# Kernel tuning notes

Measured on AMD Instinct MI355X. Metric: run time of the kernel, lower is better.

## Reference

```python
import jax, jax.numpy as jnp
import numpy as np
from jax import lax

B, W, RSS, NLED, LED_F, HID = 8192, 512, 12, 16, 8, 64


def setup_inputs() -> dict:
    key = jax.random.key(0)
    ks = jax.random.split(key, 20)
    s = 0.05
    return {
        "rss_chunk": jax.random.normal(ks[0], (B, W, RSS), jnp.float32),
        "anchor_pos": jax.random.normal(ks[1], (B, 3), jnp.float32),
        "led_feats": jax.random.normal(ks[2], (NLED, LED_F), jnp.float32),
        "led_positions": jax.random.normal(ks[3], (NLED, 3), jnp.float32),
        "freq_mask": jax.random.randint(ks[4], (RSS, NLED), 0, 2, jnp.int32),
        # temporal_conv params (torch Conv1d weight layout [out, in, k])
        "conv1_w": jax.random.normal(ks[5], (32, RSS, 3), jnp.float32) * s,
        "conv1_b": jax.random.normal(ks[6], (32,), jnp.float32) * s,
        "conv2_w": jax.random.normal(ks[7], (64, 32, 3), jnp.float32) * s,
        "conv2_b": jax.random.normal(ks[8], (64,), jnp.float32) * s,
        # projections (torch Linear weight layout [out, in])
        "q_w": jax.random.normal(ks[9], (64, W + 3), jnp.float32) * s,
        "q_b": jax.random.normal(ks[10], (64,), jnp.float32) * s,
        "k_w": jax.random.normal(ks[11], (64, LED_F + 3), jnp.float32) * s,
        "k_b": jax.random.normal(ks[12], (64,), jnp.float32) * s,
        "red_w": jax.random.normal(ks[13], (64, RSS * LED_F), jnp.float32) * s,
        "red_b": jax.random.normal(ks[14], (64,), jnp.float32) * s,
        "fus_w": jax.random.normal(ks[15], (HID, 64 + 64), jnp.float32) * s,
        "fus_b": jax.random.normal(ks[16], (HID,), jnp.float32) * s,
    }


def _conv1d(x, w, b, stride):
    # x: [B, C_in, L], w: [C_out, C_in, k], padding 1
    y = lax.conv_general_dilated(x, w, (stride,), [(1, 1)],
                                 dimension_numbers=("NCH", "OIH", "NCH"))
    return y + b[None, :, None]


def reference(rss_chunk, anchor_pos, led_feats, led_positions, freq_mask,
              conv1_w, conv1_b, conv2_w, conv2_b,
              q_w, q_b, k_w, k_b, red_w, red_b, fus_w, fus_b):
    Bc = rss_chunk.shape[0]
    x = jnp.swapaxes(rss_chunk, 1, 2)                       # [B, 12, W]

    # temporal conv branch -> [B, 64]
    h = jax.nn.relu(_conv1d(x, conv1_w, conv1_b, 1))        # [B, 32, W]
    h = jax.nn.relu(_conv1d(h, conv2_w, conv2_b, 2))        # [B, 64, W//2]
    t_feat = h.mean(axis=-1)                                # AdaptiveAvgPool1d(1)

    # queries: [B, 12, W+3] -> [B, 12, 64]
    pos_rep = jnp.broadcast_to(anchor_pos[:, None, :], (Bc, RSS, 3))
    query_in = jnp.concatenate([x, pos_rep], axis=-1)
    queries = query_in @ q_w.T + q_b

    # keys: [N, 11] -> [N, 64] (shared across batch)
    key_in = jnp.concatenate([led_feats, led_positions], axis=-1)
    keys = key_in @ k_w.T + k_b

    scores = jnp.einsum("brd,nd->brn", queries, keys)       # [B, 12, N]
    dist_sq = jnp.sum((anchor_pos[:, None, :] - led_positions[None, :, :]) ** 2, -1)
    dist_bias = 0.5 * jnp.log(1.0 / (dist_sq + 1e-8))       # [B, N]
    scores = scores + dist_bias[:, None, :]
    scores = jnp.where(freq_mask[None] == 0, jnp.finfo(scores.dtype).min, scores)

    attn = jax.nn.softmax(scores, axis=-1)                  # [B, 12, N]
    s_agg = jnp.einsum("brn,nf->brf", attn, led_feats)      # [B, 12, 8]
    s_feat = jax.nn.relu(s_agg.reshape(Bc, -1) @ red_w.T + red_b)  # [B, 64]

    combined = jnp.concatenate([t_feat, s_feat], axis=-1)   # [B, 128]
    return combined @ fus_w.T + fus_b                       # [B, hidden]
```

## Files before the change

kernel.cpp:

```cpp
#include <hip/hip_runtime.h>
#include <float.h>
#include <math.h>

typedef __bf16 bf16;
typedef __attribute__((ext_vector_type(8))) __bf16 bf16x8;
typedef __attribute__((ext_vector_type(4))) __bf16 bf16x4;
typedef __attribute__((ext_vector_type(4))) float f32x4;
typedef long long i64;

#define MK 544

#define WS_MG   0
#define WS_CVEC 17408
#define WS_W1F  17472
#define WS_W2F  21568

__device__ __forceinline__ f32x4 mfma16(bf16x8 a, bf16x8 b, f32x4 c) {
  return __builtin_amdgcn_mfma_f32_16x16x32_bf16(a, b, c, 0, 0, 0);
}
__device__ __forceinline__ f32x4 mfma8(i64 a, i64 b, f32x4 c) {
  return __builtin_amdgcn_mfma_f32_16x16x32_fp8_fp8(a, b, c, 0, 0, 0);
}

__global__ __launch_bounds__(256) void acek_pre(
    const float* __restrict__ led_feats, const float* __restrict__ led_pos,
    const float* __restrict__ q_w, const float* __restrict__ q_b,
    const float* __restrict__ k_w, const float* __restrict__ k_b,
    const float* __restrict__ c1w, const float* __restrict__ c2w,
    char* __restrict__ ws) {
  bf16* Mg = (bf16*)(ws + WS_MG);
  float* cvec = (float*)(ws + WS_CVEC);
  bf16x8* W1F = (bf16x8*)(ws + WS_W1F);
  i64* W2F = (i64*)(ws + WS_W2F);
  const int t = threadIdx.x;

  if (blockIdx.x == 34) {
    {
      int ot = t >> 7, s = (t >> 6) & 1, lane = t & 63;
      int g = lane >> 4, a15 = lane & 15;
      bf16x8 f;
#pragma unroll
      for (int j = 0; j < 8; ++j) {
        int k1 = s * 32 + g * 8 + j;
        int dk = k1 >> 4, ic = k1 & 15;
        float v = (ic < 12 && dk < 3) ? c1w[(ot * 16 + a15) * 36 + ic * 3 + dk] : 0.f;
        f[j] = (bf16)v;
      }
      W1F[t] = f;
    }
    for (int r = 0; r < 3; ++r) {
      int fi = t + r * 256;
      int o = fi / 192, rem = fi - o * 192;
      int s = rem >> 6, lane = rem & 63;
      int g = lane >> 4, a15 = lane & 15;
      float v[8];
#pragma unroll
      for (int j = 0; j < 8; ++j)
        v[j] = 16.f * c2w[(o * 16 + a15) * 96 + (g * 8 + j) * 3 + s];
      int lo = __builtin_amdgcn_cvt_pk_fp8_f32(v[0], v[1], 0, false);
      lo = __builtin_amdgcn_cvt_pk_fp8_f32(v[2], v[3], lo, true);
      int hi = __builtin_amdgcn_cvt_pk_fp8_f32(v[4], v[5], 0, false);
      hi = __builtin_amdgcn_cvt_pk_fp8_f32(v[6], v[7], hi, true);
      W2F[fi] = ((i64)(unsigned)lo) | (((i64)hi) << 32);
    }
    return;
  }

  __shared__ float keys[16 * 64];
  for (int idx = t; idx < 16 * 64; idx += 256) {
    int n = idx >> 6, d = idx & 63;
    float acc = k_b[d];
#pragma unroll
    for (int j = 0; j < 8; ++j) acc += k_w[d * 11 + j] * led_feats[n * 8 + j];
#pragma unroll
    for (int j = 0; j < 3; ++j) acc += k_w[d * 11 + 8 + j] * led_pos[n * 3 + j];
    keys[idx] = acc;
  }
  __syncthreads();
  int e = blockIdx.x * 256 + t;
  if (e < 16 * MK) {
    int n = e / MK, k = e - n * MK;
    float v = 0.f;
    if (k < 515) {
#pragma unroll 4
      for (int d = 0; d < 64; ++d) v += q_w[d * 515 + k] * keys[n * 64 + d];
    }
    Mg[e] = (bf16)v;
  }
  if (blockIdx.x == 0 && t < 16) {
    float acc = 0.f;
    for (int d = 0; d < 64; ++d) acc += q_b[d] * keys[t * 64 + d];
    cvec[t] = acc;
  }
}

__global__ __launch_bounds__(256, 4) void acek_main(
    const float* __restrict__ rss, const float* __restrict__ anchor,
    const float* __restrict__ ledf, const float* __restrict__ ledp,
    const int* __restrict__ fmask,
    const float* __restrict__ c1b, const float* __restrict__ c2b,
    const float* __restrict__ rw, const float* __restrict__ rb,
    const float* __restrict__ fw, const float* __restrict__ fb,
    const bf16* __restrict__ Mg, const float* __restrict__ cvec,
    const bf16x8* __restrict__ W1F, const i64* __restrict__ W2F,
    float* __restrict__ out) {

  __shared__ __align__(16) bf16 xw[515 * 16];
  __shared__ __align__(16) unsigned char h1[513 * 40];
  __shared__ __align__(16) float att[192];
  __shared__ __align__(16) float sagg[96];
  __shared__ __align__(16) float comb[128];
  __shared__ __align__(16) float tfp[256];

  const int tid = threadIdx.x;
  const int lane = tid & 63;
  const int wv = tid >> 6;
  const int a15 = lane & 15;
  const int g = lane >> 4;
  const int b = blockIdx.x;
  char* xwb = (char*)xw;
  char* h1b = (char*)h1;

  bf16x8 w1f[2][2];
#pragma unroll
  for (int ot = 0; ot < 2; ++ot)
#pragma unroll
    for (int s = 0; s < 2; ++s) w1f[ot][s] = W1F[(ot * 2 + s) * 64 + lane];
  i64 w2f[4][3];
#pragma unroll
  for (int o = 0; o < 4; ++o)
#pragma unroll
    for (int s = 0; s < 3; ++s) w2f[o][s] = W2F[(o * 3 + s) * 64 + lane];
  f32x4 b1v[2], b2s[4];
#pragma unroll
  for (int ot = 0; ot < 2; ++ot) b1v[ot] = *(const f32x4*)&c1b[ot * 16 + g * 4];
#pragma unroll
  for (int o = 0; o < 4; ++o) {
    f32x4 tmp = *(const f32x4*)&c2b[o * 16 + g * 4];
    b2s[o] = tmp * 16.f;
  }

  bf16x4 z4 = {(bf16)0.f, (bf16)0.f, (bf16)0.f, (bf16)0.f};
  for (int r = tid; r < 515; r += 256)
    *(bf16x4*)(xwb + r * 32 + (24 ^ ((r & 4) << 2))) = z4;
  if (tid < 12) {
    int rr = (tid >> 2) == 0 ? 0 : ((tid >> 2) == 1 ? 513 : 514);
    *(bf16x4*)(xwb + rr * 32 + (((tid & 3) * 8) ^ ((rr & 4) << 2))) = z4;
  }
  if (tid < 4) *(i64*)(h1b + tid * 8) = 0;

  const float* xb = rss + (size_t)b * 6144;
#pragma unroll
  for (int i = 0; i < 6; ++i) {
    int f = tid + i * 256;
    f32x4 v = ((const f32x4*)xb)[f];
    int e = f * 4;
    int w = e / 12;
    int c = e - w * 12;
    bf16x4 bv;
    bv[0] = (bf16)v[0]; bv[1] = (bf16)v[1]; bv[2] = (bf16)v[2]; bv[3] = (bf16)v[3];
    int row = w + 1;
    *(bf16x4*)(xwb + row * 32 + ((c * 2) ^ ((row & 4) << 2))) = bv;
  }
  __syncthreads();

  if (wv < 3) {
    const int t0 = wv * 11;
    const int tn = (wv == 2) ? 10 : 11;
    const int dk0 = g >> 1;
    const int icb16 = (g & 1) << 4;
    for (int wt = t0; wt < t0 + tn; ++wt) {
      const int wcol = wt * 16 + a15;
      f32x4 c0 = {0.f, 0.f, 0.f, 0.f}, c1 = {0.f, 0.f, 0.f, 0.f};
#pragma unroll
      for (int s = 0; s < 2; ++s) {
        int row = wcol + 2 * s + dk0;
        bf16x8 bv = *(const bf16x8*)(xwb + row * 32 + (icb16 ^ ((row & 4) << 2)));
        c0 = mfma16(w1f[0][s], bv, c0);
        c1 = mfma16(w1f[1][s], bv, c1);
      }
      const int hrow = wcol + 1;
      float v0 = fmaxf(c0[0] + b1v[0][0], 0.f), v1 = fmaxf(c0[1] + b1v[0][1], 0.f);
      float v2 = fmaxf(c0[2] + b1v[0][2], 0.f), v3 = fmaxf(c0[3] + b1v[0][3], 0.f);
      int pk0 = __builtin_amdgcn_cvt_pk_fp8_f32(v0, v1, 0, false);
      pk0 = __builtin_amdgcn_cvt_pk_fp8_f32(v2, v3, pk0, true);
      *(int*)(h1b + hrow * 40 + g * 4) = pk0;
      v0 = fmaxf(c1[0] + b1v[1][0], 0.f); v1 = fmaxf(c1[1] + b1v[1][1], 0.f);
      v2 = fmaxf(c1[2] + b1v[1][2], 0.f); v3 = fmaxf(c1[3] + b1v[1][3], 0.f);
      int pk1 = __builtin_amdgcn_cvt_pk_fp8_f32(v0, v1, 0, false);
      pk1 = __builtin_amdgcn_cvt_pk_fp8_f32(v2, v3, pk1, true);
      *(int*)(h1b + hrow * 40 + 16 + g * 4) = pk1;
    }
  } else {
    const float anc0 = anchor[(size_t)b * 3 + 0];
    const float anc1 = anchor[(size_t)b * 3 + 1];
    const float anc2 = anchor[(size_t)b * 3 + 2];
    const int rcl = (a15 < 12) ? a15 : 11;
    const bf16* MgR = Mg + a15 * MK;
    f32x4 sac = {0.f, 0.f, 0.f, 0.f};
#pragma unroll 4
    for (int s = 0; s < 16; ++s) {
      const float* xs = xb + (s * 32 + g * 8) * 12 + rcl;
      bf16x8 av;
#pragma unroll
      for (int j = 0; j < 8; ++j) av[j] = (bf16)xs[j * 12];
      bf16x8 bm = *(const bf16x8*)&MgR[s * 32 + g * 8];
      sac = mfma16(av, bm, sac);
    }
    {
      bf16x8 av = {(bf16)0.f, (bf16)0.f, (bf16)0.f, (bf16)0.f,
                   (bf16)0.f, (bf16)0.f, (bf16)0.f, (bf16)0.f};
      if (g == 0) { av[0] = (bf16)anc0; av[1] = (bf16)anc1; av[2] = (bf16)anc2; }
      bf16x8 bm = *(const bf16x8*)&MgR[512 + g * 8];
      sac = mfma16(av, bm, sac);
    }
    float dx = anc0 - ledp[a15 * 3 + 0];
    float dy = anc1 - ledp[a15 * 3 + 1];
    float dz = anc2 - ledp[a15 * 3 + 2];
    float cv = cvec[a15] - 0.5f * logf(dx * dx + dy * dy + dz * dz + 1e-8f);
#pragma unroll
    for (int rho = 0; rho < 4; ++rho) {
      int r = 4 * g + rho;
      int mrow = (r < 12) ? r : 11;
      float sc = sac[rho] + cv;
      if (fmask[mrow * 16 + a15] == 0) sc = -FLT_MAX;
      float mx = sc;
      mx = fmaxf(mx, __shfl_xor(mx, 1, 16));
      mx = fmaxf(mx, __shfl_xor(mx, 2, 16));
      mx = fmaxf(mx, __shfl_xor(mx, 4, 16));
      mx = fmaxf(mx, __shfl_xor(mx, 8, 16));
      float ev = expf(sc - mx);
      float sm = ev;
      sm += __shfl_xor(sm, 1, 16);
      sm += __shfl_xor(sm, 2, 16);
      sm += __shfl_xor(sm, 4, 16);
      sm += __shfl_xor(sm, 8, 16);
      if (r < 12) att[r * 16 + a15] = ev / sm;
    }
    for (int it = lane; it < 96; it += 64) {
      int r = it >> 3, f = it & 7;
      float acc = 0.f;
#pragma unroll
      for (int n = 0; n < 16; ++n) acc += att[r * 16 + n] * ledf[n * 8 + f];
      sagg[it] = acc;
    }
    {
      float acc = rb[lane];
      const f32x4* rwv = (const f32x4*)(rw + lane * 96);
#pragma unroll 6
      for (int i = 0; i < 24; ++i) {
        f32x4 a = rwv[i];
        f32x4 sv = *(const f32x4*)&sagg[i * 4];
        acc += a[0] * sv[0] + a[1] * sv[1] + a[2] * sv[2] + a[3] * sv[3];
      }
      comb[64 + lane] = fmaxf(acc, 0.f);
    }
  }
  __syncthreads();

  {
    float tacc[4][4] = {{0.f, 0.f, 0.f, 0.f}, {0.f, 0.f, 0.f, 0.f},
                        {0.f, 0.f, 0.f, 0.f}, {0.f, 0.f, 0.f, 0.f}};
#pragma unroll
    for (int pti = 0; pti < 4; ++pti) {
      const int p = (wv * 4 + pti) * 16 + a15;
      f32x4 cc0 = {0.f, 0.f, 0.f, 0.f}, cc1 = {0.f, 0.f, 0.f, 0.f};
      f32x4 cc2 = {0.f, 0.f, 0.f, 0.f}, cc3 = {0.f, 0.f, 0.f, 0.f};
#pragma unroll
      for (int s = 0; s < 3; ++s) {
        i64 hv = *(const i64*)(h1b + (2 * p + s) * 40 + g * 8);
        cc0 = mfma8(w2f[0][s], hv, cc0);
        cc1 = mfma8(w2f[1][s], hv, cc1);
        cc2 = mfma8(w2f[2][s], hv, cc2);
        cc3 = mfma8(w2f[3][s], hv, cc3);
      }
#pragma unroll
      for (int r = 0; r < 4; ++r) {
        tacc[0][r] += fmaxf(cc0[r] + b2s[0][r], 0.f);
        tacc[1][r] += fmaxf(cc1[r] + b2s[1][r], 0.f);
        tacc[2][r] += fmaxf(cc2[r] + b2s[2][r], 0.f);
        tacc[3][r] += fmaxf(cc3[r] + b2s[3][r], 0.f);
      }
    }
#pragma unroll
    for (int o = 0; o < 4; ++o)
#pragma unroll
      for (int r = 0; r < 4; ++r) {
        float v = tacc[o][r];
        v += __shfl_xor(v, 1, 16);
        v += __shfl_xor(v, 2, 16);
        v += __shfl_xor(v, 4, 16);
        v += __shfl_xor(v, 8, 16);
        if (a15 == 0) tfp[wv * 64 + o * 16 + g * 4 + r] = v;
      }
  }
  __syncthreads();

  if (tid < 64) {
    comb[tid] = (tfp[tid] + tfp[64 + tid] + tfp[128 + tid] + tfp[192 + tid]) *
                (1.f / 4096.f);
    float acc = fb[tid];
    const f32x4* fwv = (const f32x4*)(fw + tid * 128);
#pragma unroll 8
    for (int i = 0; i < 32; ++i) {
      f32x4 a = fwv[i];
      f32x4 c = *(const f32x4*)&comb[i * 4];
      acc += a[0] * c[0] + a[1] * c[1] + a[2] * c[2] + a[3] * c[3];
    }
    out[(size_t)b * 64 + tid] = acc;
  }
}

extern "C" void kernel_launch(void* const* d_in, const int* in_sizes, int n_in,
                              void* d_out, int out_size, void* d_ws, size_t ws_size,
                              hipStream_t stream) {
  (void)in_sizes; (void)n_in; (void)out_size; (void)ws_size;
  const float* rss   = (const float*)d_in[0];
  const float* anch  = (const float*)d_in[1];
  const float* ledf  = (const float*)d_in[2];
  const float* ledp  = (const float*)d_in[3];
  const int*   fmask = (const int*)d_in[4];
  const float* c1w = (const float*)d_in[5];
  const float* c1b = (const float*)d_in[6];
  const float* c2w = (const float*)d_in[7];
  const float* c2b = (const float*)d_in[8];
  const float* qw  = (const float*)d_in[9];
  const float* qb  = (const float*)d_in[10];
  const float* kw  = (const float*)d_in[11];
  const float* kb  = (const float*)d_in[12];
  const float* rw  = (const float*)d_in[13];
  const float* rb  = (const float*)d_in[14];
  const float* fw  = (const float*)d_in[15];
  const float* fb  = (const float*)d_in[16];
  float* outp = (float*)d_out;
  char* ws = (char*)d_ws;

  acek_pre<<<35, 256, 0, stream>>>(ledf, ledp, qw, qb, kw, kb, c1w, c2w, ws);
  acek_main<<<8192, 256, 0, stream>>>(
      rss, anch, ledf, ledp, fmask, c1b, c2b, rw, rb, fw, fb,
      (const bf16*)(ws + WS_MG), (const float*)(ws + WS_CVEC),
      (const bf16x8*)(ws + WS_W1F), (const i64*)(ws + WS_W2F), outp);
}
```

Baseline: 137.9 us.

## Rebalance conv1 tiles across waves and parallelize reduce/fusion GEMVs over all threads

Conv1 tiles are redistributed so the attention wave also handles two tiles, and waves 0-2 run a fully unrolled ten tiles each. The attention query MFMA now reads the bf16 input already staged in LDS instead of strided global loads. The reduce and fusion matvecs move from a single 64-thread wave to all 256 threads, with a 4-way split and shuffle reduction. Fast __expf and __logf replace expf and logf. The cost is an extra barrier and slightly different numerics.

```diff
diff --git a/kernel.cpp b/kernel.cpp
--- a/kernel.cpp
+++ b/kernel.cpp
@@ -154,9 +154,8 @@
   for (int i = 0; i < 6; ++i) {
     int f = tid + i * 256;
     f32x4 v = ((const f32x4*)xb)[f];
-    int e = f * 4;
-    int w = e / 12;
-    int c = e - w * 12;
+    int w = f / 3;
+    int c = (f - w * 3) * 4;
     bf16x4 bv;
     bv[0] = (bf16)v[0]; bv[1] = (bf16)v[1]; bv[2] = (bf16)v[2]; bv[3] = (bf16)v[3];
     int row = w + 1;
@@ -164,46 +163,51 @@
   }
   __syncthreads();
 
-  if (wv < 3) {
-    const int t0 = wv * 11;
-    const int tn = (wv == 2) ? 10 : 11;
+  auto conv1_tile = [&](int wt) {
     const int dk0 = g >> 1;
     const int icb16 = (g & 1) << 4;
-    for (int wt = t0; wt < t0 + tn; ++wt) {
-      const int wcol = wt * 16 + a15;
-      f32x4 c0 = {0.f, 0.f, 0.f, 0.f}, c1 = {0.f, 0.f, 0.f, 0.f};
-#pragma unroll
-      for (int s = 0; s < 2; ++s) {
-        int row = wcol + 2 * s + dk0;
-        bf16x8 bv = *(const bf16x8*)(xwb + row * 32 + (icb16 ^ ((row & 4) << 2)));
-        c0 = mfma16(w1f[0][s], bv, c0);
-        c1 = mfma16(w1f[1][s], bv, c1);
-      }
-      const int hrow = wcol + 1;
-      float v0 = fmaxf(c0[0] + b1v[0][0], 0.f), v1 = fmaxf(c0[1] + b1v[0][1], 0.f);
-      float v2 = fmaxf(c0[2] + b1v[0][2], 0.f), v3 = fmaxf(c0[3] + b1v[0][3], 0.f);
-      int pk0 = __builtin_amdgcn_cvt_pk_fp8_f32(v0, v1, 0, false);
-      pk0 = __builtin_amdgcn_cvt_pk_fp8_f32(v2, v3, pk0, true);
-      *(int*)(h1b + hrow * 40 + g * 4) = pk0;
-      v0 = fmaxf(c1[0] + b1v[1][0], 0.f); v1 = fmaxf(c1[1] + b1v[1][1], 0.f);
-      v2 = fmaxf(c1[2] + b1v[1][2], 0.f); v3 = fmaxf(c1[3] + b1v[1][3], 0.f);
-      int pk1 = __builtin_amdgcn_cvt_pk_fp8_f32(v0, v1, 0, false);
-      pk1 = __builtin_amdgcn_cvt_pk_fp8_f32(v2, v3, pk1, true);
-      *(int*)(h1b + hrow * 40 + 16 + g * 4) = pk1;
-    }
+    const int wcol = wt * 16 + a15;
+    f32x4 c0 = {0.f, 0.f, 0.f, 0.f}, c1 = {0.f, 0.f, 0.f, 0.f};
+#pragma unroll
+    for (int s = 0; s < 2; ++s) {
+      int row = wcol + 2 * s + dk0;
+      bf16x8 bv = *(const bf16x8*)(xwb + row * 32 + (icb16 ^ ((row & 4) << 2)));
+      c0 = mfma16(w1f[0][s], bv, c0);
+      c1 = mfma16(w1f[1][s], bv, c1);
+    }
+    const int hrow = wcol + 1;
+    float v0 = fmaxf(c0[0] + b1v[0][0], 0.f), v1 = fmaxf(c0[1] + b1v[0][1], 0.f);
+    float v2 = fmaxf(c0[2] + b1v[0][2], 0.f), v3 = fmaxf(c0[3] + b1v[0][3], 0.f);
+    int pk0 = __builtin_amdgcn_cvt_pk_fp8_f32(v0, v1, 0, false);
+    pk0 = __builtin_amdgcn_cvt_pk_fp8_f32(v2, v3, pk0, true);
+    *(int*)(h1b + hrow * 40 + g * 4) = pk0;
+    v0 = fmaxf(c1[0] + b1v[1][0], 0.f); v1 = fmaxf(c1[1] + b1v[1][1], 0.f);
+    v2 = fmaxf(c1[2] + b1v[1][2], 0.f); v3 = fmaxf(c1[3] + b1v[1][3], 0.f);
+    int pk1 = __builtin_amdgcn_cvt_pk_fp8_f32(v0, v1, 0, false);
+    pk1 = __builtin_amdgcn_cvt_pk_fp8_f32(v2, v3, pk1, true);
+    *(int*)(h1b + hrow * 40 + 16 + g * 4) = pk1;
+  };
+
+  if (wv < 3) {
+    const int base = wv * 10;
+#pragma unroll
+    for (int t = 0; t < 10; ++t) conv1_tile(base + t);
   } else {
+    conv1_tile(30);
+    conv1_tile(31);
     const float anc0 = anchor[(size_t)b * 3 + 0];
     const float anc1 = anchor[(size_t)b * 3 + 1];
     const float anc2 = anchor[(size_t)b * 3 + 2];
-    const int rcl = (a15 < 12) ? a15 : 11;
     const bf16* MgR = Mg + a15 * MK;
     f32x4 sac = {0.f, 0.f, 0.f, 0.f};
-#pragma unroll 4
+#pragma unroll
     for (int s = 0; s < 16; ++s) {
-      const float* xs = xb + (s * 32 + g * 8) * 12 + rcl;
       bf16x8 av;
 #pragma unroll
-      for (int j = 0; j < 8; ++j) av[j] = (bf16)xs[j * 12];
+      for (int j = 0; j < 8; ++j) {
+        int row = s * 32 + g * 8 + j + 1;
+        av[j] = *(const bf16*)(xwb + row * 32 + ((a15 * 2) ^ ((row & 4) << 2)));
+      }
       bf16x8 bm = *(const bf16x8*)&MgR[s * 32 + g * 8];
       sac = mfma16(av, bm, sac);
     }
@@ -217,7 +221,7 @@
     float dx = anc0 - ledp[a15 * 3 + 0];
     float dy = anc1 - ledp[a15 * 3 + 1];
     float dz = anc2 - ledp[a15 * 3 + 2];
-    float cv = cvec[a15] - 0.5f * logf(dx * dx + dy * dy + dz * dz + 1e-8f);
+    float cv = cvec[a15] - 0.5f * __logf(dx * dx + dy * dy + dz * dz + 1e-8f);
 #pragma unroll
     for (int rho = 0; rho < 4; ++rho) {
       int r = 4 * g + rho;
@@ -229,7 +233,7 @@
       mx = fmaxf(mx, __shfl_xor(mx, 2, 16));
       mx = fmaxf(mx, __shfl_xor(mx, 4, 16));
       mx = fmaxf(mx, __shfl_xor(mx, 8, 16));
-      float ev = expf(sc - mx);
+      float ev = __expf(sc - mx);
       float sm = ev;
       sm += __shfl_xor(sm, 1, 16);
       sm += __shfl_xor(sm, 2, 16);
@@ -243,17 +247,6 @@
 #pragma unroll
       for (int n = 0; n < 16; ++n) acc += att[r * 16 + n] * ledf[n * 8 + f];
       sagg[it] = acc;
-    }
-    {
-      float acc = rb[lane];
-      const f32x4* rwv = (const f32x4*)(rw + lane * 96);
-#pragma unroll 6
-      for (int i = 0; i < 24; ++i) {
-        f32x4 a = rwv[i];
-        f32x4 sv = *(const f32x4*)&sagg[i * 4];
-        acc += a[0] * sv[0] + a[1] * sv[1] + a[2] * sv[2] + a[3] * sv[3];
-      }
-      comb[64 + lane] = fmaxf(acc, 0.f);
     }
   }
   __syncthreads();
@@ -296,18 +289,38 @@
   }
   __syncthreads();
 
-  if (tid < 64) {
+  if (tid < 64)
     comb[tid] = (tfp[tid] + tfp[64 + tid] + tfp[128 + tid] + tfp[192 + tid]) *
                 (1.f / 4096.f);
-    float acc = fb[tid];
-    const f32x4* fwv = (const f32x4*)(fw + tid * 128);
-#pragma unroll 8
-    for (int i = 0; i < 32; ++i) {
-      f32x4 a = fwv[i];
-      f32x4 c = *(const f32x4*)&comb[i * 4];
+  {
+    const int o = tid >> 2, q = tid & 3;
+    float acc = 0.f;
+    const f32x4* rwv = (const f32x4*)(rw + o * 96 + q * 24);
+    const f32x4* sv = (const f32x4*)(sagg + q * 24);
+#pragma unroll
+    for (int i = 0; i < 6; ++i) {
+      f32x4 a = rwv[i], s = sv[i];
+      acc += a[0] * s[0] + a[1] * s[1] + a[2] * s[2] + a[3] * s[3];
+    }
+    acc += __shfl_xor(acc, 1, 4);
+    acc += __shfl_xor(acc, 2, 4);
+    if (q == 0) comb[64 + o] = fmaxf(acc + rb[o], 0.f);
+  }
+  __syncthreads();
+
+  {
+    const int o = tid >> 2, q = tid & 3;
+    float acc = 0.f;
+    const f32x4* fwv = (const f32x4*)(fw + o * 128 + q * 32);
+    const f32x4* cv = (const f32x4*)(comb + q * 32);
+#pragma unroll
+    for (int i = 0; i < 8; ++i) {
+      f32x4 a = fwv[i], c = cv[i];
       acc += a[0] * c[0] + a[1] * c[1] + a[2] * c[2] + a[3] * c[3];
     }
-    out[(size_t)b * 64 + tid] = acc;
+    acc += __shfl_xor(acc, 1, 4);
+    acc += __shfl_xor(acc, 2, 4);
+    if (q == 0) out[(size_t)b * 64 + o] = acc + fb[o];
   }
 }
 
```

Measured after the change: 147.2 us. 6.8% more time.
